# Optimization experiments

Measured on AMD Instinct MI355X. Metric: run time of the kernel, lower is better.

Reference implementation:

```python
import jax, jax.numpy as jnp
import numpy as np

E, H, I = 8, 1024, 4096
N, K = 2048, 2


def setup_inputs() -> dict:
    key = jax.random.key(0)
    ks = jax.random.split(key, 6)
    x = jax.random.normal(ks[0], (N, H), dtype=jnp.float32)
    expert_indices = jax.random.randint(ks[1], (N, K), 0, E)
    expert_weights = jax.random.uniform(ks[2], (N, K), dtype=jnp.float32)
    # kaiming-uniform style init (scale only needs to be realistic)
    b1 = float(np.sqrt(6.0 / H))
    b2 = float(np.sqrt(6.0 / I))
    w1 = jax.random.uniform(ks[3], (E, H, I), dtype=jnp.float32, minval=-b1, maxval=b1)
    w2 = jax.random.uniform(ks[4], (E, I, H), dtype=jnp.float32, minval=-b2, maxval=b2)
    w3 = jax.random.uniform(ks[5], (E, H, I), dtype=jnp.float32, minval=-b1, maxval=b1)
    return {"x": x, "expert_indices": expert_indices, "expert_weights": expert_weights,
            "w1": w1, "w2": w2, "w3": w3}


def reference(x, expert_indices, expert_weights, w1, w2, w3):
    # The torch module permutes tokens by expert, runs per-expert SwiGLU FFNs,
    # unpermutes, scales by routing weights, and sums over top_k. Mathematically:
    # out[n] = sum_k w[n,k] * FFN_{idx[n,k]}(x[n]).
    # JIT-friendly static-shape form: compute all experts densely, then gather.
    gate = jax.nn.silu(jnp.einsum('nh,ehi->nei', x, w1))   # [N,E,I]
    up = jnp.einsum('nh,ehi->nei', x, w3)                  # [N,E,I]
    y = jnp.einsum('nei,eih->neh', gate * up, w2)          # [N,E,H]
    sel = jnp.take_along_axis(y, expert_indices[:, :, None], axis=1)  # [N,K,H]
    out = jnp.sum(sel * expert_weights[:, :, None], axis=1)           # [N,H]
    return out
```

## Files before the change

kernel.cpp:

```cpp
#include <hip/hip_runtime.h>
#include <stdint.h>

#define E_NUM 8
#define H_DIM 1024
#define I_DIM 4096
#define N_TOK 2048
#define TOPK 2
#define NPAIR (N_TOK*TOPK)
#define TM 128
#define MAXSLOT (NPAIR + E_NUM*TM)
#define MAXTILE (MAXSLOT/TM)

typedef unsigned short u16;
typedef unsigned int u32;
typedef short short8 __attribute__((ext_vector_type(8)));
typedef float f32x4 __attribute__((ext_vector_type(4)));

#define OFF_W1T  ((size_t)0)
#define OFF_W3T  ((size_t)67108864)
#define OFF_W2T  ((size_t)134217728)
#define OFF_T    ((size_t)201326592)
#define OFF_Y    ((size_t)243269632)
#define OFF_XB   ((size_t)253755392)
#define OFF_META ((size_t)257949696)
#define M_TILES    0
#define M_TEXP     8
#define M_SLOTTOK  64
#define M_SLOTOF   5184
#define M_ZERO     9472
#define M_ZERO_N   544

__device__ __forceinline__ float b2f(u16 h){ return __uint_as_float(((u32)h)<<16); }
__device__ __forceinline__ u16 f2b(float f){
  u32 u = __float_as_uint(f);
  u32 r = (u + 0x7FFFu + ((u>>16)&1u)) >> 16;
  return (u16)r;
}
__device__ __forceinline__ void glds16(const void* g, void* l){
  __builtin_amdgcn_global_load_lds((const __attribute__((address_space(1))) void*)g,
                                   (__attribute__((address_space(3))) void*)l, 16, 0, 0);
}
__device__ __forceinline__ int swz_co(int chunk){
  return (((chunk >> 3) ^ chunk) & 7) * 8;
}

__global__ __launch_bounds__(256) void route_kernel(const int* __restrict__ ei,
                                                    int* __restrict__ meta){
  __shared__ int cnt[E_NUM], base_s[E_NUM], cur[E_NUM];
  int t = threadIdx.x;
  if (t < E_NUM) cnt[t] = 0;
  __syncthreads();
  for (int p = t; p < NPAIR; p += 256) atomicAdd(&cnt[ei[p]], 1);
  __syncthreads();
  if (t == 0){
    int run = 0, tile = 0;
    for (int e = 0; e < E_NUM; ++e){
      base_s[e] = run;
      int nt = (cnt[e] + TM - 1) / TM;
      for (int i = 0; i < nt; ++i) meta[M_TEXP + tile + i] = e;
      tile += nt;
      run  += nt * TM;
    }
    meta[M_TILES] = tile;
  }
  if (t < E_NUM) cur[t] = 0;
  for (int s = t; s < MAXSLOT; s += 256) meta[M_SLOTTOK + s] = -1;
  for (int z = t; z < M_ZERO_N; z += 256) meta[M_ZERO + z] = 0;
  __syncthreads();
  for (int p = t; p < NPAIR; p += 256){
    int e = ei[p];
    int r = atomicAdd(&cur[e], 1);
    int slot = base_s[e] + r;
    meta[M_SLOTTOK + slot] = p >> 1;
    meta[M_SLOTOF + p] = slot;
  }
}

__global__ __launch_bounds__(256) void castx_kernel(const float* __restrict__ x,
                                                    u16* __restrict__ xb){
  int gid = blockIdx.x * 256 + threadIdx.x;
  size_t base = (size_t)gid * 8;
  float4 a = *(const float4*)(x + base);
  float4 b = *(const float4*)(x + base + 4);
  u16 o[8] __attribute__((aligned(16)));
  o[0]=f2b(a.x); o[1]=f2b(a.y); o[2]=f2b(a.z); o[3]=f2b(a.w);
  o[4]=f2b(b.x); o[5]=f2b(b.y); o[6]=f2b(b.z); o[7]=f2b(b.w);
  *(uint4*)(void*)(xb + base) = *(const uint4*)(const void*)o;
}

__global__ __launch_bounds__(256) void transpose_kernel(const float* __restrict__ src,
                                                        u16* __restrict__ dst,
                                                        int R, int C){
  __shared__ u16 tile[128*129];
  int e  = blockIdx.z;
  int cb = blockIdx.x * 128;
  int rb = blockIdx.y * 128;
  const float* s = src + (size_t)e * R * C;
  u16* d = dst + (size_t)e * R * C;
  int tid = threadIdx.x;
  #pragma unroll
  for (int it = 0; it < 16; ++it){
    int idx = it*256 + tid;
    int row = idx >> 5, colq = (idx & 31) * 4;
    float4 v = *(const float4*)(s + (size_t)(rb+row)*C + cb + colq);
    u16* p = &tile[row*129 + colq];
    p[0]=f2b(v.x); p[1]=f2b(v.y); p[2]=f2b(v.z); p[3]=f2b(v.w);
  }
  __syncthreads();
  #pragma unroll
  for (int it = 0; it < 8; ++it){
    int idx = it*256 + tid;
    int orow = idx >> 4, oc = (idx & 15) * 8;
    u16 o[8] __attribute__((aligned(16)));
    #pragma unroll
    for (int k = 0; k < 8; ++k) o[k] = tile[(oc+k)*129 + orow];
    *(uint4*)(void*)(d + (size_t)(cb+orow)*R + rb + oc) = *(const uint4*)(const void*)o;
  }
}

__global__ __launch_bounds__(256) void ffn1_kernel(
    const u16* __restrict__ x, const u16* __restrict__ w1t, const u16* __restrict__ w3t,
    u16* __restrict__ T, const int* __restrict__ meta)
{
  const int tiles = meta[M_TILES];
  const int mt_i = blockIdx.y;
  if (mt_i >= tiles) return;
  const int e = meta[M_TEXP + mt_i];
  const int slot0 = mt_i * 128;
  const int i0 = blockIdx.x * 64;

  __shared__ u16 sA[128*64];
  __shared__ u16 sB1[64*64];
  __shared__ u16 sB3[64*64];

  const int t = threadIdx.x;
  const int lane = t & 63;
  const int wave = t >> 6;
  const int m0 = (wave >> 1) * 64;
  const int n0 = (wave & 1) * 32;
  const int lr = lane & 15;
  const int lq = lane >> 4;

  const u16* zb = (const u16*)(meta + M_ZERO);
  const u16* abase[4]; u16* aldst[4];
  #pragma unroll
  for (int r = 0; r < 4; ++r){
    int chunk = r*256 + t;
    int row = chunk >> 3;
    int co  = swz_co(chunk);
    int tok = meta[M_SLOTTOK + slot0 + row];
    abase[r] = (tok >= 0) ? (x + (size_t)tok*H_DIM + co) : (zb + co);
    aldst[r] = sA + chunk*8;
  }
  const u16* b1base[2]; const u16* b3base[2]; u16* b1dst[2]; u16* b3dst[2];
  #pragma unroll
  for (int r = 0; r < 2; ++r){
    int chunk = r*256 + t;
    int n  = chunk >> 3;
    int co = swz_co(chunk);
    size_t gb = ((size_t)e*I_DIM + i0 + n)*H_DIM + co;
    b1base[r] = w1t + gb;  b3base[r] = w3t + gb;
    b1dst[r] = sB1 + chunk*8;  b3dst[r] = sB3 + chunk*8;
  }

  f32x4 zero4 = {0.f,0.f,0.f,0.f};
  f32x4 accG[4][2], accU[4][2];
  #pragma unroll
  for (int a = 0; a < 4; ++a){
    accG[a][0]=zero4; accG[a][1]=zero4; accU[a][0]=zero4; accU[a][1]=zero4;
  }

  for (int k0 = 0; k0 < H_DIM; k0 += 64){
    #pragma unroll
    for (int r = 0; r < 4; ++r) glds16(abase[r] + k0, aldst[r]);
    #pragma unroll
    for (int r = 0; r < 2; ++r){
      glds16(b1base[r] + k0, b1dst[r]);
      glds16(b3base[r] + k0, b3dst[r]);
    }
    __syncthreads();
    #pragma unroll
    for (int ks = 0; ks < 64; ks += 32){
      const int sx = ((ks >> 3) + lq) ^ (lr & 7);
      short8 af[4];
      #pragma unroll
      for (int m = 0; m < 4; ++m)
        af[m] = *(const short8*)(const void*)(sA + (m0 + m*16 + lr)*64 + sx*8);
      #pragma unroll
      for (int n = 0; n < 2; ++n){
        short8 bg = *(const short8*)(const void*)(sB1 + (n0 + n*16 + lr)*64 + sx*8);
        short8 bu = *(const short8*)(const void*)(sB3 + (n0 + n*16 + lr)*64 + sx*8);
        #pragma unroll
        for (int m = 0; m < 4; ++m){
          accG[m][n] = __builtin_amdgcn_mfma_f32_16x16x32_bf16(af[m], bg, accG[m][n], 0,0,0);
          accU[m][n] = __builtin_amdgcn_mfma_f32_16x16x32_bf16(af[m], bu, accU[m][n], 0,0,0);
        }
      }
    }
    __syncthreads();
  }

  #pragma unroll
  for (int m = 0; m < 4; ++m)
  #pragma unroll
  for (int n = 0; n < 2; ++n)
  #pragma unroll
  for (int r = 0; r < 4; ++r){
    int row = m0 + m*16 + lq*4 + r;
    int col = i0 + n0 + n*16 + lr;
    float g = accG[m][n][r];
    float u = accU[m][n][r];
    float val = (g / (1.0f + __expf(-g))) * u;
    T[(size_t)(slot0 + row)*I_DIM + col] = f2b(val);
  }
}

__global__ __launch_bounds__(256) void ffn2_kernel(
    const u16* __restrict__ T, const u16* __restrict__ w2t,
    u16* __restrict__ Y, const int* __restrict__ meta)
{
  const int tiles = meta[M_TILES];
  const int mt_i = blockIdx.y;
  if (mt_i >= tiles) return;
  const int e = meta[M_TEXP + mt_i];
  const int slot0 = mt_i * 128;
  const int h0 = blockIdx.x * 64;

  __shared__ u16 sA[128*64];
  __shared__ u16 sB[64*64];

  const int t = threadIdx.x;
  const int lane = t & 63;
  const int wave = t >> 6;
  const int m0 = (wave >> 1) * 64;
  const int n0 = (wave & 1) * 32;
  const int lr = lane & 15;
  const int lq = lane >> 4;

  const u16* abase[4]; u16* aldst[4];
  #pragma unroll
  for (int r = 0; r < 4; ++r){
    int chunk = r*256 + t;
    int row = chunk >> 3;
    int co  = swz_co(chunk);
    abase[r] = T + (size_t)(slot0 + row)*I_DIM + co;
    aldst[r] = sA + chunk*8;
  }
  const u16* bbase[2]; u16* bdst[2];
  #pragma unroll
  for (int r = 0; r < 2; ++r){
    int chunk = r*256 + t;
    int n  = chunk >> 3;
    int co = swz_co(chunk);
    bbase[r] = w2t + ((size_t)e*H_DIM + h0 + n)*I_DIM + co;
    bdst[r] = sB + chunk*8;
  }

  f32x4 zero4 = {0.f,0.f,0.f,0.f};
  f32x4 acc[4][2];
  #pragma unroll
  for (int a = 0; a < 4; ++a){ acc[a][0]=zero4; acc[a][1]=zero4; }

  for (int k0 = 0; k0 < I_DIM; k0 += 64){
    #pragma unroll
    for (int r = 0; r < 4; ++r) glds16(abase[r] + k0, aldst[r]);
    #pragma unroll
    for (int r = 0; r < 2; ++r) glds16(bbase[r] + k0, bdst[r]);
    __syncthreads();
    #pragma unroll
    for (int ks = 0; ks < 64; ks += 32){
      const int sx = ((ks >> 3) + lq) ^ (lr & 7);
      short8 af[4];
      #pragma unroll
      for (int m = 0; m < 4; ++m)
        af[m] = *(const short8*)(const void*)(sA + (m0 + m*16 + lr)*64 + sx*8);
      #pragma unroll
      for (int n = 0; n < 2; ++n){
        short8 bf = *(const short8*)(const void*)(sB + (n0 + n*16 + lr)*64 + sx*8);
        #pragma unroll
        for (int m = 0; m < 4; ++m)
          acc[m][n] = __builtin_amdgcn_mfma_f32_16x16x32_bf16(af[m], bf, acc[m][n], 0,0,0);
      }
    }
    __syncthreads();
  }

  #pragma unroll
  for (int m = 0; m < 4; ++m)
  #pragma unroll
  for (int n = 0; n < 2; ++n)
  #pragma unroll
  for (int r = 0; r < 4; ++r){
    int row = m0 + m*16 + lq*4 + r;
    int col = h0 + n0 + n*16 + lr;
    Y[(size_t)(slot0 + row)*H_DIM + col] = f2b(acc[m][n][r]);
  }
}

__global__ __launch_bounds__(256) void combine_kernel(
    const u16* __restrict__ Y, const float* __restrict__ ew,
    const int* __restrict__ meta, float* __restrict__ out)
{
  int gid = blockIdx.x * 256 + threadIdx.x;
  int n  = gid >> 7;
  int hc = (gid & 127) * 8;
  int s0 = meta[M_SLOTOF + n*2];
  int s1 = meta[M_SLOTOF + n*2 + 1];
  float w0 = ew[n*2];
  float w1v = ew[n*2 + 1];
  const short8 y0 = *(const short8*)(const void*)(Y + (size_t)s0*H_DIM + hc);
  const short8 y1 = *(const short8*)(const void*)(Y + (size_t)s1*H_DIM + hc);
  float o[8];
  #pragma unroll
  for (int j = 0; j < 8; ++j)
    o[j] = w0 * b2f((u16)y0[j]) + w1v * b2f((u16)y1[j]);
  float4* outv = (float4*)(out + (size_t)n*H_DIM + hc);
  outv[0] = *(float4*)(void*)&o[0];
  outv[1] = *(float4*)(void*)&o[4];
}

extern "C" void kernel_launch(void* const* d_in, const int* in_sizes, int n_in,
                              void* d_out, int out_size, void* d_ws, size_t ws_size,
                              hipStream_t stream)
{
  const float* x  = (const float*)d_in[0];
  const int*   ei = (const int*)d_in[1];
  const float* ew = (const float*)d_in[2];
  const float* w1 = (const float*)d_in[3];
  const float* w2 = (const float*)d_in[4];
  const float* w3 = (const float*)d_in[5];
  float* out = (float*)d_out;
  char* ws = (char*)d_ws;
  u16* w1t = (u16*)(ws + OFF_W1T);
  u16* w3t = (u16*)(ws + OFF_W3T);
  u16* w2t = (u16*)(ws + OFF_W2T);
  u16* Tb  = (u16*)(ws + OFF_T);
  u16* Yb  = (u16*)(ws + OFF_Y);
  u16* xb  = (u16*)(ws + OFF_XB);
  int* meta = (int*)(ws + OFF_META);

  route_kernel<<<1, 256, 0, stream>>>(ei, meta);
  castx_kernel<<<dim3((N_TOK*H_DIM/8)/256), 256, 0, stream>>>(x, xb);
  transpose_kernel<<<dim3(I_DIM/128, H_DIM/128, E_NUM), 256, 0, stream>>>(w1, w1t, H_DIM, I_DIM);
  transpose_kernel<<<dim3(I_DIM/128, H_DIM/128, E_NUM), 256, 0, stream>>>(w3, w3t, H_DIM, I_DIM);
  transpose_kernel<<<dim3(H_DIM/128, I_DIM/128, E_NUM), 256, 0, stream>>>(w2, w2t, I_DIM, H_DIM);
  ffn1_kernel<<<dim3(I_DIM/64, MAXTILE), 256, 0, stream>>>(xb, w1t, w3t, Tb, meta);
  ffn2_kernel<<<dim3(H_DIM/64, MAXTILE), 256, 0, stream>>>(Tb, w2t, Yb, meta);
  combine_kernel<<<dim3((N_TOK*H_DIM/8)/256), 256, 0, stream>>>(Yb, ew, meta, out);
}
```

Measured before the change: 605.9 us.

## Widen FFN GEMM tiles to 128 columns and merge w1/w3 transposes

Both FFN GEMM kernels now compute 128x128 output tiles instead of 128x64, so each wave holds a 64x64 sub-tile. That doubles the MFMA work per loaded A fragment and halves the number of A-tile reloads from global memory. The w1 and w3 weight transposes are merged into a single launch to cut one kernel dispatch. In exchange, ffn1 needs more registers (64 accumulator vectors) and more LDS, which may lower occupancy, and there are fewer blocks, which may hurt load balance.

After: 664.0 us. +9.6%, slower.

```diff
diff --git a/kernel.cpp b/kernel.cpp
--- a/kernel.cpp
+++ b/kernel.cpp
@@ -118,6 +118,39 @@
   }
 }
 
+__global__ __launch_bounds__(256) void transpose2_kernel(const float* __restrict__ s1,
+                                                         const float* __restrict__ s3,
+                                                         u16* __restrict__ d1,
+                                                         u16* __restrict__ d3,
+                                                         int R, int C){
+  __shared__ u16 tile[128*129];
+  int which = blockIdx.z >> 3;
+  int e  = blockIdx.z & 7;
+  int cb = blockIdx.x * 128;
+  int rb = blockIdx.y * 128;
+  const float* s = (which ? s3 : s1) + (size_t)e * R * C;
+  u16* d = (which ? d3 : d1) + (size_t)e * R * C;
+  int tid = threadIdx.x;
+  #pragma unroll
+  for (int it = 0; it < 16; ++it){
+    int idx = it*256 + tid;
+    int row = idx >> 5, colq = (idx & 31) * 4;
+    float4 v = *(const float4*)(s + (size_t)(rb+row)*C + cb + colq);
+    u16* p = &tile[row*129 + colq];
+    p[0]=f2b(v.x); p[1]=f2b(v.y); p[2]=f2b(v.z); p[3]=f2b(v.w);
+  }
+  __syncthreads();
+  #pragma unroll
+  for (int it = 0; it < 8; ++it){
+    int idx = it*256 + tid;
+    int orow = idx >> 4, oc = (idx & 15) * 8;
+    u16 o[8] __attribute__((aligned(16)));
+    #pragma unroll
+    for (int k = 0; k < 8; ++k) o[k] = tile[(oc+k)*129 + orow];
+    *(uint4*)(void*)(d + (size_t)(cb+orow)*R + rb + oc) = *(const uint4*)(const void*)o;
+  }
+}
+
 __global__ __launch_bounds__(256) void ffn1_kernel(
     const u16* __restrict__ x, const u16* __restrict__ w1t, const u16* __restrict__ w3t,
     u16* __restrict__ T, const int* __restrict__ meta)
@@ -127,17 +160,17 @@
   if (mt_i >= tiles) return;
   const int e = meta[M_TEXP + mt_i];
   const int slot0 = mt_i * 128;
-  const int i0 = blockIdx.x * 64;
+  const int i0 = blockIdx.x * 128;
 
   __shared__ u16 sA[128*64];
-  __shared__ u16 sB1[64*64];
-  __shared__ u16 sB3[64*64];
+  __shared__ u16 sB1[128*64];
+  __shared__ u16 sB3[128*64];
 
   const int t = threadIdx.x;
   const int lane = t & 63;
   const int wave = t >> 6;
   const int m0 = (wave >> 1) * 64;
-  const int n0 = (wave & 1) * 32;
+  const int n0 = (wave & 1) * 64;
   const int lr = lane & 15;
   const int lq = lane >> 4;
 
@@ -152,9 +185,9 @@
     abase[r] = (tok >= 0) ? (x + (size_t)tok*H_DIM + co) : (zb + co);
     aldst[r] = sA + chunk*8;
   }
-  const u16* b1base[2]; const u16* b3base[2]; u16* b1dst[2]; u16* b3dst[2];
-  #pragma unroll
-  for (int r = 0; r < 2; ++r){
+  const u16* b1base[4]; const u16* b3base[4]; u16* b1dst[4]; u16* b3dst[4];
+  #pragma unroll
+  for (int r = 0; r < 4; ++r){
     int chunk = r*256 + t;
     int n  = chunk >> 3;
     int co = swz_co(chunk);
@@ -164,17 +197,17 @@
   }
 
   f32x4 zero4 = {0.f,0.f,0.f,0.f};
-  f32x4 accG[4][2], accU[4][2];
-  #pragma unroll
-  for (int a = 0; a < 4; ++a){
-    accG[a][0]=zero4; accG[a][1]=zero4; accU[a][0]=zero4; accU[a][1]=zero4;
-  }
+  f32x4 accG[4][4], accU[4][4];
+  #pragma unroll
+  for (int a = 0; a < 4; ++a)
+  #pragma unroll
+  for (int b = 0; b < 4; ++b){ accG[a][b]=zero4; accU[a][b]=zero4; }
 
   for (int k0 = 0; k0 < H_DIM; k0 += 64){
     #pragma unroll
     for (int r = 0; r < 4; ++r) glds16(abase[r] + k0, aldst[r]);
     #pragma unroll
-    for (int r = 0; r < 2; ++r){
+    for (int r = 0; r < 4; ++r){
       glds16(b1base[r] + k0, b1dst[r]);
       glds16(b3base[r] + k0, b3dst[r]);
     }
@@ -187,7 +220,7 @@
       for (int m = 0; m < 4; ++m)
         af[m] = *(const short8*)(const void*)(sA + (m0 + m*16 + lr)*64 + sx*8);
       #pragma unroll
-      for (int n = 0; n < 2; ++n){
+      for (int n = 0; n < 4; ++n){
         short8 bg = *(const short8*)(const void*)(sB1 + (n0 + n*16 + lr)*64 + sx*8);
         short8 bu = *(const short8*)(const void*)(sB3 + (n0 + n*16 + lr)*64 + sx*8);
         #pragma unroll
@@ -203,7 +236,7 @@
   #pragma unroll
   for (int m = 0; m < 4; ++m)
   #pragma unroll
-  for (int n = 0; n < 2; ++n)
+  for (int n = 0; n < 4; ++n)
   #pragma unroll
   for (int r = 0; r < 4; ++r){
     int row = m0 + m*16 + lq*4 + r;
@@ -224,16 +257,16 @@
   if (mt_i >= tiles) return;
   const int e = meta[M_TEXP + mt_i];
   const int slot0 = mt_i * 128;
-  const int h0 = blockIdx.x * 64;
+  const int h0 = blockIdx.x * 128;
 
   __shared__ u16 sA[128*64];
-  __shared__ u16 sB[64*64];
+  __shared__ u16 sB[128*64];
 
   const int t = threadIdx.x;
   const int lane = t & 63;
   const int wave = t >> 6;
   const int m0 = (wave >> 1) * 64;
-  const int n0 = (wave & 1) * 32;
+  const int n0 = (wave & 1) * 64;
   const int lr = lane & 15;
   const int lq = lane >> 4;
 
@@ -246,9 +279,9 @@
     abase[r] = T + (size_t)(slot0 + row)*I_DIM + co;
     aldst[r] = sA + chunk*8;
   }
-  const u16* bbase[2]; u16* bdst[2];
-  #pragma unroll
-  for (int r = 0; r < 2; ++r){
+  const u16* bbase[4]; u16* bdst[4];
+  #pragma unroll
+  for (int r = 0; r < 4; ++r){
     int chunk = r*256 + t;
     int n  = chunk >> 3;
     int co = swz_co(chunk);
@@ -257,15 +290,17 @@
   }
 
   f32x4 zero4 = {0.f,0.f,0.f,0.f};
-  f32x4 acc[4][2];
-  #pragma unroll
-  for (int a = 0; a < 4; ++a){ acc[a][0]=zero4; acc[a][1]=zero4; }
+  f32x4 acc[4][4];
+  #pragma unroll
+  for (int a = 0; a < 4; ++a)
+  #pragma unroll
+  for (int b = 0; b < 4; ++b) acc[a][b]=zero4;
 
   for (int k0 = 0; k0 < I_DIM; k0 += 64){
     #pragma unroll
     for (int r = 0; r < 4; ++r) glds16(abase[r] + k0, aldst[r]);
     #pragma unroll
-    for (int r = 0; r < 2; ++r) glds16(bbase[r] + k0, bdst[r]);
+    for (int r = 0; r < 4; ++r) glds16(bbase[r] + k0, bdst[r]);
     __syncthreads();
     #pragma unroll
     for (int ks = 0; ks < 64; ks += 32){
@@ -275,7 +310,7 @@
       for (int m = 0; m < 4; ++m)
         af[m] = *(const short8*)(const void*)(sA + (m0 + m*16 + lr)*64 + sx*8);
       #pragma unroll
-      for (int n = 0; n < 2; ++n){
+      for (int n = 0; n < 4; ++n){
         short8 bf = *(const short8*)(const void*)(sB + (n0 + n*16 + lr)*64 + sx*8);
         #pragma unroll
         for (int m = 0; m < 4; ++m)
@@ -288,7 +323,7 @@
   #pragma unroll
   for (int m = 0; m < 4; ++m)
   #pragma unroll
-  for (int n = 0; n < 2; ++n)
+  for (int n = 0; n < 4; ++n)
   #pragma unroll
   for (int r = 0; r < 4; ++r){
     int row = m0 + m*16 + lq*4 + r;
@@ -341,10 +376,9 @@
 
   route_kernel<<<1, 256, 0, stream>>>(ei, meta);
   castx_kernel<<<dim3((N_TOK*H_DIM/8)/256), 256, 0, stream>>>(x, xb);
-  transpose_kernel<<<dim3(I_DIM/128, H_DIM/128, E_NUM), 256, 0, stream>>>(w1, w1t, H_DIM, I_DIM);
-  transpose_kernel<<<dim3(I_DIM/128, H_DIM/128, E_NUM), 256, 0, stream>>>(w3, w3t, H_DIM, I_DIM);
+  transpose2_kernel<<<dim3(I_DIM/128, H_DIM/128, 2*E_NUM), 256, 0, stream>>>(w1, w3, w1t, w3t, H_DIM, I_DIM);
   transpose_kernel<<<dim3(H_DIM/128, I_DIM/128, E_NUM), 256, 0, stream>>>(w2, w2t, I_DIM, H_DIM);
-  ffn1_kernel<<<dim3(I_DIM/64, MAXTILE), 256, 0, stream>>>(xb, w1t, w3t, Tb, meta);
-  ffn2_kernel<<<dim3(H_DIM/64, MAXTILE), 256, 0, stream>>>(Tb, w2t, Yb, meta);
+  ffn1_kernel<<<dim3(I_DIM/128, MAXTILE), 256, 0, stream>>>(xb, w1t, w3t, Tb, meta);
+  ffn2_kernel<<<dim3(H_DIM/128, MAXTILE), 256, 0, stream>>>(Tb, w2t, Yb, meta);
   combine_kernel<<<dim3((N_TOK*H_DIM/8)/256), 256, 0, stream>>>(Yb, ew, meta, out);
 }
```
